# Kernel optimization log

Hardware: AMD Instinct MI355X
Metric: run time of the kernel (lower is better)

The kernel has to match this reference:

```python
import jax, jax.numpy as jnp
import numpy as np

DT, TAU_S, TAU_M = 1.0, 4.0, 20.0
ALPHA = float(np.exp(-DT / TAU_S))   # synaptic current decay
BETA = float(np.exp(-DT / TAU_M))    # membrane potential decay
THRESH = 1.0
STEPS, BATCH, D1, D2 = 128, 256, 1024, 1024


def setup_inputs() -> dict:
    key = jax.random.key(0)
    k1, k2 = jax.random.split(key)
    inp = jax.random.uniform(k1, (STEPS, BATCH, D1), dtype=jnp.float32)
    # kaiming_normal_ on (d2, d1): std = sqrt(2 / fan_in), mu = 1.0
    weight = jax.random.normal(k2, (D2, D1), dtype=jnp.float32) * np.sqrt(2.0 / D1)
    return {"input": inp, "weight": weight}


def reference(input, weight):
    steps, batch = input.shape[0], input.shape[1]
    d2 = weight.shape[0]
    # Step i uses input[i-1]; precompute all linear projections at once.
    lin = jnp.einsum('tbi,oi->tbo', input[:-1], weight)  # [steps-1, B, d2]

    def step(carry, cur):
        syn, mem = carry
        # snntorch Synaptic, reset_mechanism='zero': reset from PREVIOUS mem
        reset = (mem > THRESH).astype(mem.dtype)
        syn = ALPHA * syn + cur
        mem = (BETA * mem + syn) * (1.0 - reset)
        spk = (mem > THRESH).astype(mem.dtype)
        return (syn, mem), (spk, mem, syn)

    init = (jnp.zeros((batch, d2), input.dtype), jnp.zeros((batch, d2), input.dtype))
    _, (spk, V, I) = jax.lax.scan(step, init, lin)
    z = jnp.zeros((1, batch, d2), input.dtype)  # step 0 stays zero
    output = jnp.concatenate([z, spk], axis=0)
    V = jnp.concatenate([z, V], axis=0)
    I = jnp.concatenate([z, I], axis=0)
    return output, V, I
```

## Files before the change

### kernel.cpp

```cpp
#include <hip/hip_runtime.h>
#include <hip/hip_fp16.h>


#define STEPS 128
#define BATCH 256
#define DIN   1024
#define DOUT  1024

#define ALPHA 0.7788007830714049f
#define BETA  0.9512294245007140f

constexpr int    GM      = (STEPS - 1) * BATCH;
constexpr size_t PLANE   = (size_t)BATCH * DOUT;
constexpr size_t A_ELEMS = (size_t)GM * DIN;
constexpr size_t W_ELEMS = (size_t)DOUT * DIN;

constexpr int NKT = 96;

typedef __attribute__((ext_vector_type(8))) _Float16 half8;
typedef __attribute__((ext_vector_type(4))) float float4v;

__global__ __launch_bounds__(256)
void split_kernel(const float* __restrict__ x,
                  unsigned short* __restrict__ hi,
                  unsigned short* __restrict__ lo)
{
    const size_t i = (size_t)blockIdx.x * 256 + threadIdx.x;
    const float4 v = reinterpret_cast<const float4*>(x)[i];
    float f[4] = {v.x, v.y, v.z, v.w};
    unsigned short hb[4], lb[4];
#pragma unroll
    for (int j = 0; j < 4; ++j) {
        _Float16 h = (_Float16)f[j];
        _Float16 l = (_Float16)(f[j] - (float)h);
        hb[j] = *reinterpret_cast<unsigned short*>(&h);
        lb[j] = *reinterpret_cast<unsigned short*>(&l);
    }
    ushort4 hv = {hb[0], hb[1], hb[2], hb[3]};
    ushort4 lv = {lb[0], lb[1], lb[2], lb[3]};
    reinterpret_cast<ushort4*>(hi)[i] = hv;
    reinterpret_cast<ushort4*>(lo)[i] = lv;
}

__device__ __forceinline__ void load16(const unsigned short* g, unsigned short* l)
{
    __builtin_amdgcn_global_load_lds(
        (const __attribute__((address_space(1))) void*)g,
        (__attribute__((address_space(3))) void*)l, 16, 0, 0);
}

__global__ __launch_bounds__(512, 2)
void gemm_kernel(const unsigned short* __restrict__ Ah,
                 const unsigned short* __restrict__ Al,
                 const unsigned short* __restrict__ Wh,
                 const unsigned short* __restrict__ Wl,
                 float* __restrict__ C)
{
    __shared__ __align__(16) unsigned short smem[65536];

    const int lin = blockIdx.x;
    const int xcd = lin & 7, slot = lin >> 3;
    const int mp  = xcd * 16 + (slot >> 2);
    const int nt  = slot & 3;
    if (mp >= GM / 256) return;
    const int m0 = mp * 256;
    const int n0 = nt * 256;

    const int t = threadIdx.x;
    const int w = t >> 6, l = t & 63;
    const int wr = w >> 2, wc = w & 3;
    const int lr = l & 15, q = l >> 4;

    const int swz = q ^ ((l >> 1) & 3);

    const int laneA = (wr * 128 + lr) * 32 + swz * 8;
    const int laneB = (wc * 64  + lr) * 32 + swz * 8;

    const int srow = l >> 2;
    const int sg   = ((l & 3) ^ ((l >> 3) & 3)) * 8;

    const size_t sA0 = (size_t)(m0 + w * 32 +      srow) * DIN + sg;
    const size_t sA1 = (size_t)(m0 + w * 32 + 16 + srow) * DIN + sg;
    const size_t sB0 = (size_t)(n0 + w * 32 +      srow) * DIN + sg;
    const size_t sB1 = (size_t)(n0 + w * 32 + 16 + srow) * DIN + sg;

    unsigned short* dA0 = smem + w * 1024;
    unsigned short* dA1 = smem + w * 1024 + 512;
    unsigned short* dB0 = smem + 32768 + w * 1024;
    unsigned short* dB1 = smem + 32768 + w * 1024 + 512;

    auto STAGE = [&](int ks) {
        const int p  = ks >> 5;
        const int kk = (ks & 31) << 5;
        const unsigned short* sa = (p == 1) ? Al : Ah;
        const unsigned short* sw = (p == 2) ? Wl : Wh;
        const int bo = (ks & 3) * 8192;
        load16(sa + sA0 + kk, dA0 + bo);
        load16(sa + sA1 + kk, dA1 + bo);
        load16(sw + sB0 + kk, dB0 + bo);
        load16(sw + sB1 + kk, dB1 + bo);
    };

    float4v acc[8][4];
#pragma unroll
    for (int m = 0; m < 8; ++m)
#pragma unroll
        for (int n = 0; n < 4; ++n)
            acc[m][n] = (float4v){0.f, 0.f, 0.f, 0.f};

    STAGE(0); STAGE(1); STAGE(2);
    asm volatile("s_waitcnt vmcnt(8)" ::: "memory");
    __builtin_amdgcn_s_barrier();

    for (int kt = 0; kt < NKT; ++kt) {
        const int bo = (kt & 3) * 8192;
        const unsigned short* pA = smem + bo + laneA;
        const unsigned short* pB = smem + 32768 + bo + laneB;

        half8 a[8], b[4];
#pragma unroll
        for (int m = 0; m < 8; ++m)
            a[m] = *reinterpret_cast<const half8*>(pA + m * 512);
#pragma unroll
        for (int n = 0; n < 4; ++n)
            b[n] = *reinterpret_cast<const half8*>(pB + n * 512);

        int ks = kt + 3;
        if (ks >= NKT) ks -= NKT;
        STAGE(ks);

        __builtin_amdgcn_s_setprio(1);
#pragma unroll
        for (int m = 0; m < 8; ++m)
#pragma unroll
            for (int n = 0; n < 4; ++n)
                acc[m][n] = __builtin_amdgcn_mfma_f32_16x16x32_f16(
                    a[m], b[n], acc[m][n], 0, 0, 0);
        __builtin_amdgcn_s_setprio(0);

        asm volatile("s_waitcnt vmcnt(8)" ::: "memory");
        __builtin_amdgcn_s_barrier();
    }

    const int mw = m0 + wr * 128 + q * 4;
    const int nw = n0 + wc * 64 + lr;
#pragma unroll
    for (int m = 0; m < 8; ++m)
#pragma unroll
        for (int n = 0; n < 4; ++n)
#pragma unroll
            for (int rg = 0; rg < 4; ++rg)
                C[(size_t)(mw + m * 16 + rg) * DOUT + (nw + n * 16)] = acc[m][n][rg];
}

__global__ __launch_bounds__(256)
void scan_kernel(float* __restrict__ out)
{
    const int idx = blockIdx.x * 256 + threadIdx.x;
    float* o0 = out;
    float* o1 = out + STEPS * PLANE;
    float* o2 = out + 2 * STEPS * PLANE;

    __builtin_nontemporal_store(0.0f, &o0[idx]);
    __builtin_nontemporal_store(0.0f, &o1[idx]);
    __builtin_nontemporal_store(0.0f, &o2[idx]);

    float n1 = o2[idx + PLANE];
    float n2 = o2[idx + 2 * PLANE];
    float n3 = o2[idx + 3 * PLANE];

    float syn = 0.0f, mem = 0.0f;
    size_t off = idx;
    for (int i = 1; i < STEPS; ++i) {
        off += PLANE;
        const float cur = n1; n1 = n2; n2 = n3;
        if (i + 3 < STEPS) n3 = o2[off + 3 * PLANE];
        const float reset = (mem > 1.0f) ? 1.0f : 0.0f;
        syn = ALPHA * syn + cur;
        mem = (BETA * mem + syn) * (1.0f - reset);
        const float spk = (mem > 1.0f) ? 1.0f : 0.0f;
        __builtin_nontemporal_store(spk, &o0[off]);
        __builtin_nontemporal_store(mem, &o1[off]);
        __builtin_nontemporal_store(syn, &o2[off]);
    }
}

extern "C" void kernel_launch(void* const* d_in, const int* in_sizes, int n_in,
                              void* d_out, int out_size, void* d_ws, size_t ws_size,
                              hipStream_t stream)
{
    const float* input  = (const float*)d_in[0];
    const float* weight = (const float*)d_in[1];
    float* out = (float*)d_out;

    unsigned short* Ah = (unsigned short*)out;
    unsigned short* Al = Ah + A_ELEMS;
    unsigned short* Wh = (unsigned short*)(out + STEPS * PLANE);
    unsigned short* Wl = Wh + W_ELEMS;
    float* lin = out + 2 * STEPS * PLANE + PLANE;

    split_kernel<<<(int)(A_ELEMS / 1024), 256, 0, stream>>>(input, Ah, Al);
    split_kernel<<<(int)(W_ELEMS / 1024), 256, 0, stream>>>(weight, Wh, Wl);

    gemm_kernel<<<512, 512, 0, stream>>>(Ah, Al, Wh, Wl, lin);

    scan_kernel<<<(int)(PLANE / 256), 256, 0, stream>>>(out);
}
```

Before: 690.2 us.

## Load hi/lo A and W tiles together per k-step to reuse fragments across split products

The GEMM K loop changes from 96 sequential passes (Ah*Wh, Al*Wh, Ah*Wl over K) to 32 passes. Each pass stages the hi and lo halves of both A and W into a double-buffered LDS tile. The three split-precision MFMA groups then run back to back, reusing the loaded A-hi and W-hi fragments and using explicit ds_read and waitcnt scheduling. The aim is to cut redundant global and LDS traffic for re-reading the hi operands. In exchange, the pipeline drops from three stages in flight to double buffering with a full vmcnt(0) wait each iteration, which may expose global load latency.

```diff
diff --git a/kernel.cpp b/kernel.cpp
--- a/kernel.cpp
+++ b/kernel.cpp
@@ -14,8 +14,6 @@
 constexpr size_t PLANE   = (size_t)BATCH * DOUT;
 constexpr size_t A_ELEMS = (size_t)GM * DIN;
 constexpr size_t W_ELEMS = (size_t)DOUT * DIN;
-
-constexpr int NKT = 96;
 
 typedef __attribute__((ext_vector_type(8))) _Float16 half8;
 typedef __attribute__((ext_vector_type(4))) float float4v;
@@ -49,6 +47,13 @@
         (__attribute__((address_space(3))) void*)l, 16, 0, 0);
 }
 
+__device__ __forceinline__ half8 ldsr(unsigned addr)
+{
+    half8 r;
+    asm volatile("ds_read_b128 %0, %1" : "=v"(r) : "v"(addr) : "memory");
+    return r;
+}
+
 __global__ __launch_bounds__(512, 2)
 void gemm_kernel(const unsigned short* __restrict__ Ah,
                  const unsigned short* __restrict__ Al,
@@ -73,8 +78,8 @@
 
     const int swz = q ^ ((l >> 1) & 3);
 
-    const int laneA = (wr * 128 + lr) * 32 + swz * 8;
-    const int laneB = (wc * 64  + lr) * 32 + swz * 8;
+    const unsigned rdA = (unsigned)((wr * 128 + lr) * 64 + swz * 16);
+    const unsigned rdB = (unsigned)(32768 + (wc * 64 + lr) * 64 + swz * 16);
 
     const int srow = l >> 2;
     const int sg   = ((l & 3) ^ ((l >> 3) & 3)) * 8;
@@ -84,21 +89,17 @@
     const size_t sB0 = (size_t)(n0 + w * 32 +      srow) * DIN + sg;
     const size_t sB1 = (size_t)(n0 + w * 32 + 16 + srow) * DIN + sg;
 
-    unsigned short* dA0 = smem + w * 1024;
-    unsigned short* dA1 = smem + w * 1024 + 512;
-    unsigned short* dB0 = smem + 32768 + w * 1024;
-    unsigned short* dB1 = smem + 32768 + w * 1024 + 512;
-
     auto STAGE = [&](int ks) {
-        const int p  = ks >> 5;
         const int kk = (ks & 31) << 5;
-        const unsigned short* sa = (p == 1) ? Al : Ah;
-        const unsigned short* sw = (p == 2) ? Wl : Wh;
-        const int bo = (ks & 3) * 8192;
-        load16(sa + sA0 + kk, dA0 + bo);
-        load16(sa + sA1 + kk, dA1 + bo);
-        load16(sw + sB0 + kk, dB0 + bo);
-        load16(sw + sB1 + kk, dB1 + bo);
+        unsigned short* d = smem + ((ks & 1) << 15) + w * 1024;
+        load16(Ah + sA0 + kk, d);
+        load16(Ah + sA1 + kk, d + 512);
+        load16(Al + sA0 + kk, d + 8192);
+        load16(Al + sA1 + kk, d + 8704);
+        load16(Wh + sB0 + kk, d + 16384);
+        load16(Wh + sB1 + kk, d + 16896);
+        load16(Wl + sB0 + kk, d + 24576);
+        load16(Wl + sB1 + kk, d + 25088);
     };
 
     float4v acc[8][4];
@@ -108,37 +109,59 @@
         for (int n = 0; n < 4; ++n)
             acc[m][n] = (float4v){0.f, 0.f, 0.f, 0.f};
 
-    STAGE(0); STAGE(1); STAGE(2);
-    asm volatile("s_waitcnt vmcnt(8)" ::: "memory");
+    STAGE(0);
+    asm volatile("s_waitcnt vmcnt(0)" ::: "memory");
     __builtin_amdgcn_s_barrier();
 
-    for (int kt = 0; kt < NKT; ++kt) {
-        const int bo = (kt & 3) * 8192;
-        const unsigned short* pA = smem + bo + laneA;
-        const unsigned short* pB = smem + 32768 + bo + laneB;
-
-        half8 a[8], b[4];
-#pragma unroll
-        for (int m = 0; m < 8; ++m)
-            a[m] = *reinterpret_cast<const half8*>(pA + m * 512);
-#pragma unroll
-        for (int n = 0; n < 4; ++n)
-            b[n] = *reinterpret_cast<const half8*>(pB + n * 512);
-
-        int ks = kt + 3;
-        if (ks >= NKT) ks -= NKT;
-        STAGE(ks);
-
+    for (int kt = 0; kt < 32; ++kt) {
+        const unsigned sb = (unsigned)((kt & 1) << 16);
+
+        STAGE((kt + 1) & 31);
+
+        half8 ah[8], bh[4], bl[4];
+
+#pragma unroll
+        for (int m = 0; m < 8; ++m) ah[m] = ldsr(sb + rdA + m * 1024);
+#pragma unroll
+        for (int n = 0; n < 4; ++n) bh[n] = ldsr(sb + rdB + n * 1024);
+        asm volatile("s_waitcnt lgkmcnt(0)" ::: "memory");
+        __builtin_amdgcn_sched_barrier(0);
         __builtin_amdgcn_s_setprio(1);
 #pragma unroll
         for (int m = 0; m < 8; ++m)
 #pragma unroll
             for (int n = 0; n < 4; ++n)
                 acc[m][n] = __builtin_amdgcn_mfma_f32_16x16x32_f16(
-                    a[m], b[n], acc[m][n], 0, 0, 0);
+                    ah[m], bh[n], acc[m][n], 0, 0, 0);
         __builtin_amdgcn_s_setprio(0);
 
-        asm volatile("s_waitcnt vmcnt(8)" ::: "memory");
+#pragma unroll
+        for (int n = 0; n < 4; ++n) bl[n] = ldsr(sb + rdB + 16384 + n * 1024);
+        asm volatile("s_waitcnt lgkmcnt(0)" ::: "memory");
+        __builtin_amdgcn_sched_barrier(0);
+        __builtin_amdgcn_s_setprio(1);
+#pragma unroll
+        for (int m = 0; m < 8; ++m)
+#pragma unroll
+            for (int n = 0; n < 4; ++n)
+                acc[m][n] = __builtin_amdgcn_mfma_f32_16x16x32_f16(
+                    ah[m], bl[n], acc[m][n], 0, 0, 0);
+        __builtin_amdgcn_s_setprio(0);
+
+#pragma unroll
+        for (int m = 0; m < 8; ++m) ah[m] = ldsr(sb + rdA + 16384 + m * 1024);
+        asm volatile("s_waitcnt lgkmcnt(0)" ::: "memory");
+        __builtin_amdgcn_sched_barrier(0);
+        __builtin_amdgcn_s_setprio(1);
+#pragma unroll
+        for (int m = 0; m < 8; ++m)
+#pragma unroll
+            for (int n = 0; n < 4; ++n)
+                acc[m][n] = __builtin_amdgcn_mfma_f32_16x16x32_f16(
+                    ah[m], bh[n], acc[m][n], 0, 0, 0);
+        __builtin_amdgcn_s_setprio(0);
+
+        asm volatile("s_waitcnt vmcnt(0)" ::: "memory");
         __builtin_amdgcn_s_barrier();
     }
 
```

After: 686.5 us. Within noise of the previous version (-0.5%).
